# Kernel tuning notes

Measured on AMD Instinct MI355X. Metric: run time of the kernel, lower is better.

The kernel has to match this reference:

```python
import jax, jax.numpy as jnp
import numpy as np

N_NODES = 100000
N_EDGES = 3200000
N_GRAPHS = 1024
IN_DIM, HID, OUT = 1, 32, 32
BN_EPS = 1e-5


def setup_inputs() -> dict:
    key = jax.random.key(0)
    ks = jax.random.split(key, 12)
    inp = {
        "x": jax.random.normal(ks[0], (N_NODES, IN_DIM), dtype=jnp.float32),
        "edge_index": jax.random.randint(ks[1], (2, N_EDGES), 0, N_NODES, dtype=jnp.int64),
        "batch": jnp.sort(jax.random.randint(ks[2], (N_NODES,), 0, N_GRAPHS, dtype=jnp.int64)),
        # GCNConv linear weights (out = x @ W + b) and BatchNorm (eval-mode) params
        "W1": jax.random.normal(ks[3], (IN_DIM, HID), dtype=jnp.float32) / np.sqrt(IN_DIM),
        "b1": jnp.zeros((HID,), jnp.float32),
        "bn1_g": jnp.ones((HID,), jnp.float32),
        "bn1_b": jnp.zeros((HID,), jnp.float32),
        "bn1_m": jax.random.normal(ks[4], (HID,), dtype=jnp.float32) * 0.1,
        "bn1_v": jnp.ones((HID,), jnp.float32),
        "W2": jax.random.normal(ks[5], (HID, HID), dtype=jnp.float32) / np.sqrt(HID),
        "b2": jnp.zeros((HID,), jnp.float32),
        "bn2_g": jnp.ones((HID,), jnp.float32),
        "bn2_b": jnp.zeros((HID,), jnp.float32),
        "bn2_m": jax.random.normal(ks[6], (HID,), dtype=jnp.float32) * 0.1,
        "bn2_v": jnp.ones((HID,), jnp.float32),
        "W3": jax.random.normal(ks[7], (HID, OUT), dtype=jnp.float32) / np.sqrt(HID),
        "b3": jnp.zeros((OUT,), jnp.float32),
    }
    return inp


def _gcn_norm(edge_index, n_nodes):
    # add self loops, compute sym-normalized edge weights (PyG GCNConv default)
    loop = jnp.arange(n_nodes, dtype=edge_index.dtype)
    src = jnp.concatenate([edge_index[0], loop])
    dst = jnp.concatenate([edge_index[1], loop])
    deg = jax.ops.segment_sum(jnp.ones_like(dst, dtype=jnp.float32), dst, num_segments=n_nodes)
    dinv = jnp.where(deg > 0, jax.lax.rsqrt(deg), 0.0)
    norm = dinv[src] * dinv[dst]  # [E + N]
    return src, dst, norm


def _gcn_conv(x, src, dst, norm, W, b, n_nodes):
    h = x @ W                                   # [N, F_out]
    msg = h[src] * norm[:, None]                # gather + scale, [E+N, F_out]
    out = jax.ops.segment_sum(msg, dst, num_segments=n_nodes)  # scatter-add
    return out + b


def _bn_eval(x, g, b, m, v):
    return (x - m) * jax.lax.rsqrt(v + BN_EPS) * g + b


def reference(x, edge_index, batch, W1, b1, bn1_g, bn1_b, bn1_m, bn1_v,
              W2, b2, bn2_g, bn2_b, bn2_m, bn2_v, W3, b3):
    n = x.shape[0]
    src, dst, norm = _gcn_norm(edge_index, n)
    h = _gcn_conv(x, src, dst, norm, W1, b1, n)
    h = jax.nn.relu(_bn_eval(h, bn1_g, bn1_b, bn1_m, bn1_v))  # dropout = id (eval)
    h = _gcn_conv(h, src, dst, norm, W2, b2, n)
    h = jax.nn.relu(_bn_eval(h, bn2_g, bn2_b, bn2_m, bn2_v))
    h = _gcn_conv(h, src, dst, norm, W3, b3, n)
    # global mean pool over graphs
    sums = jax.ops.segment_sum(h, batch, num_segments=N_GRAPHS)
    cnts = jax.ops.segment_sum(jnp.ones((n,), h.dtype), batch, num_segments=N_GRAPHS)
    return sums / jnp.maximum(cnts, 1.0)[:, None]
```

## Files before the change

### kernel.cpp

```cpp
#include <hip/hip_runtime.h>

#define N_NODES 100000
#define N_EDGES 3200000
#define N_GRAPHS 1024
#define HID 32
#define BN_EPS 1e-5f
#define NB 256

#define NBKT 512
#define NPB 196
#define PART_TILE 4096
#define PART_THREADS 256
#define PART_EPT (PART_TILE / PART_THREADS)

#define G2_NODES 8
#define G2_WCAP 2048


__device__ __forceinline__ int lbound(const int* __restrict__ a, int n, int key) {
    int lo = 0, hi = n;
    while (lo < hi) {
        int mid = (lo + hi) >> 1;
        if (a[mid] < key) lo = mid + 1; else hi = mid;
    }
    return lo;
}

__device__ __forceinline__ float bf2f(unsigned short h) {
    return __uint_as_float((unsigned)h << 16);
}
__device__ __forceinline__ unsigned short f2bf(float x) {
    unsigned u = __float_as_uint(x);
    u += 0x7fffu + ((u >> 16) & 1u);
    return (unsigned short)(u >> 16);
}


__global__ void k_zero(int* __restrict__ bhist) {
    bhist[threadIdx.x] = 0;
}

__global__ void k_hist(const int* __restrict__ dst, int* __restrict__ bhist) {
    __shared__ int h[NBKT];
    for (int i = threadIdx.x; i < NBKT; i += NB) h[i] = 0;
    __syncthreads();
    for (int e = blockIdx.x * NB + threadIdx.x; e < N_EDGES; e += gridDim.x * NB)
        atomicAdd(&h[__builtin_nontemporal_load(&dst[e]) / NPB], 1);
    __syncthreads();
    for (int i = threadIdx.x; i < NBKT; i += NB)
        if (h[i]) atomicAdd(&bhist[i], h[i]);
}

__global__ void k_scan512(const int* __restrict__ bhist, int* __restrict__ bstart,
                          int* __restrict__ bcursor) {
    __shared__ int sm[NBKT];
    int t = threadIdx.x;
    int orig = bhist[t];
    sm[t] = orig;
    __syncthreads();
    for (int off = 1; off < NBKT; off <<= 1) {
        int v = (t >= off) ? sm[t - off] : 0;
        __syncthreads();
        sm[t] += v;
        __syncthreads();
    }
    int ex = sm[t] - orig;
    bstart[t] = ex;
    bcursor[t] = ex;
    if (t == NBKT - 1) bstart[NBKT] = sm[t];
}

__global__ void k_partition(const int* __restrict__ src, const int* __restrict__ dst,
                            int* __restrict__ bcursor, unsigned* __restrict__ ebuf) {
    __shared__ int lh[NBKT];
    __shared__ int lcur[NBKT];
    const int tile0 = blockIdx.x * PART_TILE;
    for (int i = threadIdx.x; i < NBKT; i += PART_THREADS) lh[i] = 0;
    __syncthreads();
    int s[PART_EPT], bk[PART_EPT], dl[PART_EPT];
#pragma unroll
    for (int k = 0; k < PART_EPT; ++k) {
        int e = tile0 + k * PART_THREADS + threadIdx.x;
        bool ok = (e < N_EDGES);
        int sv = ok ? __builtin_nontemporal_load(&src[e]) : 0;
        int dv = ok ? __builtin_nontemporal_load(&dst[e]) : 0;
        s[k] = sv;
        bk[k] = ok ? (dv / NPB) : -1;
        dl[k] = dv - bk[k] * NPB;
        if (ok) atomicAdd(&lh[bk[k]], 1);
    }
    __syncthreads();
    for (int i = threadIdx.x; i < NBKT; i += PART_THREADS)
        lcur[i] = lh[i] ? atomicAdd(&bcursor[i], lh[i]) : 0;
    __syncthreads();
#pragma unroll
    for (int k = 0; k < PART_EPT; ++k) {
        if (bk[k] >= 0) {
            int pos = atomicAdd(&lcur[bk[k]], 1);
            ebuf[pos] = ((unsigned)dl[k] << 17) | (unsigned)s[k];
        }
    }
}

__global__ void k_bucket(const int* __restrict__ bstart,
                         const unsigned* __restrict__ ebuf,
                         const float* __restrict__ x,
                         int* __restrict__ rowstart, int* __restrict__ deg,
                         float* __restrict__ dinv, float* __restrict__ zs1,
                         int* __restrict__ csr) {
    __shared__ int hist[NPB];
    __shared__ int sm[256];
    __shared__ int lcur[NPB];
    const int b = blockIdx.x;
    const int node0 = b * NPB;
    const int nn = N_NODES - node0;
    const int elo = bstart[b], ehi = bstart[b + 1];
    const int t = threadIdx.x;

    for (int i = t; i < NPB; i += blockDim.x) hist[i] = 0;
    __syncthreads();
    for (int e = elo + t; e < ehi; e += blockDim.x)
        atomicAdd(&hist[ebuf[e] >> 17], 1);
    __syncthreads();
    int orig = 0;
    if (t < 256) { orig = (t < NPB) ? hist[t] : 0; sm[t] = orig; }
    __syncthreads();
    for (int off = 1; off < 256; off <<= 1) {
        int v = 0;
        if (t < 256 && t >= off) v = sm[t - off];
        __syncthreads();
        if (t < 256) sm[t] += v;
        __syncthreads();
    }
    if (t < NPB) {
        int ex = sm[t] - orig;
        lcur[t] = ex;
        if (t < nn) {
            int node = node0 + t;
            rowstart[node] = elo + ex;
            deg[node] = orig;
            float di = rsqrtf((float)(orig + 1));
            dinv[node] = di;
            zs1[node] = di * x[node];
        }
    }
    __syncthreads();
    for (int e = elo + t; e < ehi; e += blockDim.x) {
        unsigned pk = ebuf[e];
        int pos = atomicAdd(&lcur[pk >> 17], 1);
        csr[elo + pos] = (int)(pk & 0x1FFFFu);
    }
}


__global__ void k_gather1(const int* __restrict__ rowstart, const int* __restrict__ deg,
                          const int* __restrict__ csr, const float* __restrict__ dinv,
                          const float* __restrict__ zs1, float2* __restrict__ sd) {
    int v = blockIdx.x * NB + threadIdx.x;
    if (v < N_NODES) {
        int lo = rowstart[v], n = deg[v];
        float acc = zs1[v];
        int j = 0;
        for (; j + 4 <= n; j += 4) {
            int u0 = __builtin_nontemporal_load(&csr[lo + j]);
            int u1 = __builtin_nontemporal_load(&csr[lo + j + 1]);
            int u2 = __builtin_nontemporal_load(&csr[lo + j + 2]);
            int u3 = __builtin_nontemporal_load(&csr[lo + j + 3]);
            float a0 = zs1[u0], a1 = zs1[u1], a2 = zs1[u2], a3 = zs1[u3];
            acc += (a0 + a1) + (a2 + a3);
        }
        for (; j < n; ++j) acc += zs1[csr[lo + j]];
        float di = dinv[v];
        sd[v] = make_float2(di * acc, di);
    }
}

__global__ void k_gather2(const int* __restrict__ rowstart, const int* __restrict__ deg,
                          const int* __restrict__ csr, const float2* __restrict__ sd,
                          const float* __restrict__ W1, const float* __restrict__ b1,
                          const float* __restrict__ g1, const float* __restrict__ bb1,
                          const float* __restrict__ m1, const float* __restrict__ v1,
                          const float* __restrict__ W2,
                          const float* __restrict__ b2, const float* __restrict__ g2,
                          const float* __restrict__ bb2, const float* __restrict__ m2,
                          const float* __restrict__ v2,
                          unsigned short* __restrict__ zs3a,
                          unsigned short* __restrict__ zs3b) {
    __shared__ float Ws[HID * HID];
    __shared__ float2 sde[G2_WCAP];
    __shared__ float rowbuf[G2_NODES][HID + 1];
    __shared__ int sb[2];
    const int tid = threadIdx.x;
    for (int k = tid; k < HID * HID; k += NB) Ws[k] = W2[k];

    const int r = tid >> 5, f = tid & 31;
    const int v = blockIdx.x * G2_NODES + r;
    const bool valid = v < N_NODES;

    if (tid == 0) {
        int first = blockIdx.x * G2_NODES;
        int last = min(first + G2_NODES - 1, N_NODES - 1);
        sb[0] = rowstart[first];
        sb[1] = rowstart[last] + deg[last];
    }

    const float sc1 = g1[f] * rsqrtf(v1[f] + BN_EPS);
    const float A = W1[f] * sc1;
    const float Bc = (b1[f] - m1[f]) * sc1 + bb1[f];

    float di = 0.0f, acc = 0.0f;
    int rs = 0, re = 0;
    if (valid) {
        rs = rowstart[v];
        re = rs + deg[v];
        float2 pv = sd[v];
        di = pv.y;
        acc = di * fmaxf(pv.x * A + Bc, 0.0f);
    }
    __syncthreads();
    const int blo = sb[0], bhi = sb[1];

    for (int w = blo; w < bhi; w += G2_WCAP) {
        const int wn = min(G2_WCAP, bhi - w);
        for (int i = tid; i < wn; i += NB) {
            int u = __builtin_nontemporal_load(&csr[w + i]);
            sde[i] = sd[u];
        }
        __syncthreads();
        int jlo = max(rs, w) - w;
        int jhi = min(re, w + wn) - w;
        int j = jlo;
        for (; j + 4 <= jhi; j += 4) {
            float2 p0 = sde[j], p1 = sde[j + 1], p2 = sde[j + 2], p3 = sde[j + 3];
            float a0 = p0.y * fmaxf(p0.x * A + Bc, 0.0f);
            float a1 = p1.y * fmaxf(p1.x * A + Bc, 0.0f);
            float a2 = p2.y * fmaxf(p2.x * A + Bc, 0.0f);
            float a3 = p3.y * fmaxf(p3.x * A + Bc, 0.0f);
            acc += (a0 + a1) + (a2 + a3);
        }
        for (; j < jhi; ++j) {
            float2 p = sde[j];
            acc += p.y * fmaxf(p.x * A + Bc, 0.0f);
        }
        __syncthreads();
    }
    acc *= di;
    rowbuf[r][f] = acc;
    __syncthreads();
    if (valid) {
        float h = b2[f];
#pragma unroll
        for (int k = 0; k < HID; ++k) h += rowbuf[r][k] * Ws[k * HID + f];
        float sc2 = g2[f] * rsqrtf(v2[f] + BN_EPS);
        float z = fmaxf((h - m2[f]) * sc2 + bb2[f], 0.0f);
        unsigned short o = f2bf(di * z);
        if (f < 16) zs3a[v * 16 + f] = o;
        else        zs3b[v * 16 + (f - 16)] = o;
    }
}


__global__ void k_gather3h(const int* __restrict__ rowstart, const int* __restrict__ deg,
                           const int* __restrict__ csr, const float* __restrict__ dinv,
                           const unsigned short* __restrict__ tab,
                           unsigned short* __restrict__ agg3h, int halfofs) {
    int t = blockIdx.x * NB + threadIdx.x;
    int v = t >> 4, f = t & 15;
    if (v < N_NODES) {
        int lo = rowstart[v], n = deg[v];
        float acc = bf2f(tab[v * 16 + f]);
        int j = 0;
        for (; j + 8 <= n; j += 8) {
            int u0 = __builtin_nontemporal_load(&csr[lo + j]);
            int u1 = __builtin_nontemporal_load(&csr[lo + j + 1]);
            int u2 = __builtin_nontemporal_load(&csr[lo + j + 2]);
            int u3 = __builtin_nontemporal_load(&csr[lo + j + 3]);
            int u4 = __builtin_nontemporal_load(&csr[lo + j + 4]);
            int u5 = __builtin_nontemporal_load(&csr[lo + j + 5]);
            int u6 = __builtin_nontemporal_load(&csr[lo + j + 6]);
            int u7 = __builtin_nontemporal_load(&csr[lo + j + 7]);
            float a0 = bf2f(tab[u0 * 16 + f]);
            float a1 = bf2f(tab[u1 * 16 + f]);
            float a2 = bf2f(tab[u2 * 16 + f]);
            float a3 = bf2f(tab[u3 * 16 + f]);
            float a4 = bf2f(tab[u4 * 16 + f]);
            float a5 = bf2f(tab[u5 * 16 + f]);
            float a6 = bf2f(tab[u6 * 16 + f]);
            float a7 = bf2f(tab[u7 * 16 + f]);
            acc += ((a0 + a1) + (a2 + a3)) + ((a4 + a5) + (a6 + a7));
        }
        for (; j < n; ++j) acc += bf2f(tab[csr[lo + j] * 16 + f]);
        __builtin_nontemporal_store(f2bf(dinv[v] * acc), &agg3h[v * HID + halfofs + f]);
    }
}


__global__ void k_pool(const unsigned short* __restrict__ agg3h,
                       const int* __restrict__ batch,
                       const float* __restrict__ W3, const float* __restrict__ b3,
                       float* __restrict__ out) {
    __shared__ float Ws[HID * HID];
    __shared__ float part[NB / HID][HID + 1];
    __shared__ float mrow[HID];
    int g = blockIdx.x;
    for (int k = threadIdx.x; k < HID * HID; k += NB) Ws[k] = W3[k];

    int lo = lbound(batch, N_NODES, g);
    int hi = lbound(batch, N_NODES, g + 1);

    int r = threadIdx.x >> 5, f = threadIdx.x & 31;
    float acc = 0.0f;
    for (int i = lo + r; i < hi; i += NB / HID)
        acc += bf2f(__builtin_nontemporal_load(&agg3h[i * HID + f]));
    part[r][f] = acc;
    __syncthreads();
    if (threadIdx.x < HID) {
        float srow = 0.0f;
#pragma unroll
        for (int k = 0; k < NB / HID; ++k) srow += part[k][threadIdx.x];
        float c = (float)(hi - lo);
        mrow[threadIdx.x] = (hi > lo) ? srow / c : 0.0f;
    }
    __syncthreads();
    if (threadIdx.x < HID) {
        int ff = threadIdx.x;
        float o = 0.0f;
        if (hi > lo) {
            o = b3[ff];
#pragma unroll
            for (int k = 0; k < HID; ++k) o += mrow[k] * Ws[k * HID + ff];
        }
        out[g * HID + ff] = o;
    }
}


extern "C" void kernel_launch(void* const* d_in, const int* in_sizes, int n_in,
                              void* d_out, int out_size, void* d_ws, size_t ws_size,
                              hipStream_t stream) {
    const float* x     = (const float*)d_in[0];
    const int*   eidx  = (const int*)d_in[1];
    const int*   batch = (const int*)d_in[2];
    const float* W1    = (const float*)d_in[3];
    const float* b1    = (const float*)d_in[4];
    const float* bn1g  = (const float*)d_in[5];
    const float* bn1b  = (const float*)d_in[6];
    const float* bn1m  = (const float*)d_in[7];
    const float* bn1v  = (const float*)d_in[8];
    const float* W2    = (const float*)d_in[9];
    const float* b2    = (const float*)d_in[10];
    const float* bn2g  = (const float*)d_in[11];
    const float* bn2b  = (const float*)d_in[12];
    const float* bn2m  = (const float*)d_in[13];
    const float* bn2v  = (const float*)d_in[14];
    const float* W3    = (const float*)d_in[15];
    const float* b3    = (const float*)d_in[16];
    float* out = (float*)d_out;

    const int* src = eidx;
    const int* dst = eidx + N_EDGES;

    char* ws = (char*)d_ws;
    size_t off = 0;
    auto carve = [&](size_t bytes) {
        void* p = ws + off;
        off += (bytes + 255) & ~size_t(255);
        return p;
    };
    int*    bhist    = (int*)carve(NBKT * 4);
    int*    bstart   = (int*)carve((NBKT + 1) * 4);
    int*    bcursor  = (int*)carve(NBKT * 4);
    int*    rowstart = (int*)carve(N_NODES * 4);
    int*    deg      = (int*)carve(N_NODES * 4);
    float*  dinv     = (float*)carve(N_NODES * 4);
    float*  zs1      = (float*)carve(N_NODES * 4);
    float2* sd       = (float2*)carve((size_t)N_NODES * 8);
    int*    csr      = (int*)carve((size_t)N_EDGES * 4);
    char*   region   = (char*)carve((size_t)N_EDGES * 4);
    unsigned*       ebuf  = (unsigned*)region;
    unsigned short* zs3a  = (unsigned short*)region;
    unsigned short* zs3b  = (unsigned short*)(region + (size_t)N_NODES * 16 * 2);
    unsigned short* agg3h = (unsigned short*)(region + (size_t)N_NODES * 32 * 2);

    const int gN    = (N_NODES + NB - 1) / NB;
    const int gG2   = (N_NODES + G2_NODES - 1) / G2_NODES;
    const int gG3   = (N_NODES * 16 + NB - 1) / NB;
    const int gPart = (N_EDGES + PART_TILE - 1) / PART_TILE;

    k_zero<<<1, NBKT, 0, stream>>>(bhist);
    k_hist<<<1024, NB, 0, stream>>>(dst, bhist);
    k_scan512<<<1, NBKT, 0, stream>>>(bhist, bstart, bcursor);
    k_partition<<<gPart, PART_THREADS, 0, stream>>>(src, dst, bcursor, ebuf);
    k_bucket<<<NBKT, 512, 0, stream>>>(bstart, ebuf, x, rowstart, deg, dinv, zs1, csr);
    k_gather1<<<gN, NB, 0, stream>>>(rowstart, deg, csr, dinv, zs1, sd);
    k_gather2<<<gG2, NB, 0, stream>>>(rowstart, deg, csr, sd,
                                      W1, b1, bn1g, bn1b, bn1m, bn1v,
                                      W2, b2, bn2g, bn2b, bn2m, bn2v, zs3a, zs3b);
    k_gather3h<<<gG3, NB, 0, stream>>>(rowstart, deg, csr, dinv, zs3a, agg3h, 0);
    k_gather3h<<<gG3, NB, 0, stream>>>(rowstart, deg, csr, dinv, zs3b, agg3h, 16);
    k_pool<<<N_GRAPHS, NB, 0, stream>>>(agg3h, batch, W3, b3, out);
}
```

Measured before the change: 267.4 us.

## Split edge lists across sub-groups per node in gather2 and gather3h

In k_gather2 each node now gets a full 64-lane wavefront instead of 32 threads, with the two half-waves splitting the node's edges and the 32x32 matvec. The partials are combined with a cross-lane shuffle, and the edge window and nodes per block are halved. In k_gather3h each node gets a 64-lane wavefront where four 16-lane groups stride the edge list, and the partials are reduced with shuffles. The aim is to shorten per-thread serial loops over edges and put more independent loads in flight, in exchange for four times as many blocks and some reduction overhead.

```diff
diff --git a/kernel.cpp b/kernel.cpp
--- a/kernel.cpp
+++ b/kernel.cpp
@@ -13,8 +13,8 @@
 #define PART_THREADS 256
 #define PART_EPT (PART_TILE / PART_THREADS)
 
-#define G2_NODES 8
-#define G2_WCAP 2048
+#define G2_NODES 4
+#define G2_WCAP 1024
 
 
 __device__ __forceinline__ int lbound(const int* __restrict__ a, int n, int key) {
@@ -193,7 +193,10 @@
     const int tid = threadIdx.x;
     for (int k = tid; k < HID * HID; k += NB) Ws[k] = W2[k];
 
-    const int r = tid >> 5, f = tid & 31;
+    const int r = tid >> 6;
+    const int lane = tid & 63;
+    const int f = lane & 31;
+    const int esub = lane >> 5;
     const int v = blockIdx.x * G2_NODES + r;
     const bool valid = v < N_NODES;
 
@@ -215,7 +218,7 @@
         re = rs + deg[v];
         float2 pv = sd[v];
         di = pv.y;
-        acc = di * fmaxf(pv.x * A + Bc, 0.0f);
+        if (esub == 0) acc = di * fmaxf(pv.x * A + Bc, 0.0f);
     }
     __syncthreads();
     const int blo = sb[0], bhi = sb[1];
@@ -229,28 +232,34 @@
         __syncthreads();
         int jlo = max(rs, w) - w;
         int jhi = min(re, w + wn) - w;
-        int j = jlo;
-        for (; j + 4 <= jhi; j += 4) {
-            float2 p0 = sde[j], p1 = sde[j + 1], p2 = sde[j + 2], p3 = sde[j + 3];
-            float a0 = p0.y * fmaxf(p0.x * A + Bc, 0.0f);
-            float a1 = p1.y * fmaxf(p1.x * A + Bc, 0.0f);
-            float a2 = p2.y * fmaxf(p2.x * A + Bc, 0.0f);
-            float a3 = p3.y * fmaxf(p3.x * A + Bc, 0.0f);
-            acc += (a0 + a1) + (a2 + a3);
-        }
-        for (; j < jhi; ++j) {
-            float2 p = sde[j];
-            acc += p.y * fmaxf(p.x * A + Bc, 0.0f);
-        }
-        __syncthreads();
-    }
+        int jb = jlo;
+        for (; jb + 4 <= jhi; jb += 4) {
+            float2 p0 = sde[jb + esub];
+            float2 p1 = sde[jb + 2 + esub];
+            acc += p0.y * fmaxf(p0.x * A + Bc, 0.0f);
+            acc += p1.y * fmaxf(p1.x * A + Bc, 0.0f);
+        }
+        for (; jb < jhi; jb += 2) {
+            int j = jb + esub;
+            if (j < jhi) {
+                float2 p = sde[j];
+                acc += p.y * fmaxf(p.x * A + Bc, 0.0f);
+            }
+        }
+        __syncthreads();
+    }
+    acc += __shfl_xor(acc, 32, 64);
     acc *= di;
-    rowbuf[r][f] = acc;
-    __syncthreads();
-    if (valid) {
-        float h = b2[f];
+    if (lane < 32) rowbuf[r][f] = acc;
+    __syncthreads();
+
+    float hp = 0.0f;
+    const int k0 = esub * 16;
 #pragma unroll
-        for (int k = 0; k < HID; ++k) h += rowbuf[r][k] * Ws[k * HID + f];
+    for (int k = 0; k < 16; ++k) hp += rowbuf[r][k0 + k] * Ws[(k0 + k) * HID + f];
+    hp += __shfl_xor(hp, 32, 64);
+    if (valid && lane < 32) {
+        float h = b2[f] + hp;
         float sc2 = g2[f] * rsqrtf(v2[f] + BN_EPS);
         float z = fmaxf((h - m2[f]) * sc2 + bb2[f], 0.0f);
         unsigned short o = f2bf(di * z);
@@ -259,38 +268,45 @@
     }
 }
 
-
 __global__ void k_gather3h(const int* __restrict__ rowstart, const int* __restrict__ deg,
                            const int* __restrict__ csr, const float* __restrict__ dinv,
                            const unsigned short* __restrict__ tab,
                            unsigned short* __restrict__ agg3h, int halfofs) {
-    int t = blockIdx.x * NB + threadIdx.x;
-    int v = t >> 4, f = t & 15;
-    if (v < N_NODES) {
-        int lo = rowstart[v], n = deg[v];
-        float acc = bf2f(tab[v * 16 + f]);
-        int j = 0;
-        for (; j + 8 <= n; j += 8) {
-            int u0 = __builtin_nontemporal_load(&csr[lo + j]);
-            int u1 = __builtin_nontemporal_load(&csr[lo + j + 1]);
-            int u2 = __builtin_nontemporal_load(&csr[lo + j + 2]);
-            int u3 = __builtin_nontemporal_load(&csr[lo + j + 3]);
-            int u4 = __builtin_nontemporal_load(&csr[lo + j + 4]);
-            int u5 = __builtin_nontemporal_load(&csr[lo + j + 5]);
-            int u6 = __builtin_nontemporal_load(&csr[lo + j + 6]);
-            int u7 = __builtin_nontemporal_load(&csr[lo + j + 7]);
-            float a0 = bf2f(tab[u0 * 16 + f]);
-            float a1 = bf2f(tab[u1 * 16 + f]);
-            float a2 = bf2f(tab[u2 * 16 + f]);
-            float a3 = bf2f(tab[u3 * 16 + f]);
-            float a4 = bf2f(tab[u4 * 16 + f]);
-            float a5 = bf2f(tab[u5 * 16 + f]);
-            float a6 = bf2f(tab[u6 * 16 + f]);
-            float a7 = bf2f(tab[u7 * 16 + f]);
-            acc += ((a0 + a1) + (a2 + a3)) + ((a4 + a5) + (a6 + a7));
-        }
-        for (; j < n; ++j) acc += bf2f(tab[csr[lo + j] * 16 + f]);
-        __builtin_nontemporal_store(f2bf(dinv[v] * acc), &agg3h[v * HID + halfofs + f]);
+    const int tid = threadIdx.x;
+    const int lane = tid & 63;
+    const int f = lane & 15;
+    const int esub = lane >> 4;
+    const int v = blockIdx.x * 4 + (tid >> 6);
+    if (v >= N_NODES) return;
+
+    const int lo = rowstart[v], n = deg[v];
+    float acc = 0.0f;
+    int jb = 0;
+    for (; jb + 16 <= n; jb += 16) {
+        int j0 = jb + esub, j1 = jb + 4 + esub, j2 = jb + 8 + esub, j3 = jb + 12 + esub;
+        int u0 = __builtin_nontemporal_load(&csr[lo + j0]);
+        int u1 = __builtin_nontemporal_load(&csr[lo + j1]);
+        int u2 = __builtin_nontemporal_load(&csr[lo + j2]);
+        int u3 = __builtin_nontemporal_load(&csr[lo + j3]);
+        float a0 = bf2f(tab[u0 * 16 + f]);
+        float a1 = bf2f(tab[u1 * 16 + f]);
+        float a2 = bf2f(tab[u2 * 16 + f]);
+        float a3 = bf2f(tab[u3 * 16 + f]);
+        acc += (a0 + a1) + (a2 + a3);
+    }
+    for (; jb < n; jb += 4) {
+        int j = jb + esub;
+        if (j < n) {
+            int u = __builtin_nontemporal_load(&csr[lo + j]);
+            acc += bf2f(tab[u * 16 + f]);
+        }
+    }
+    acc += __shfl_xor(acc, 16, 64);
+    acc += __shfl_xor(acc, 32, 64);
+    if (esub == 0) {
+        acc += bf2f(tab[v * 16 + f]);
+        __builtin_nontemporal_store(f2bf(dinv[v] * acc),
+                                    &agg3h[v * HID + halfofs + f]);
     }
 }
 
@@ -384,7 +400,7 @@
 
     const int gN    = (N_NODES + NB - 1) / NB;
     const int gG2   = (N_NODES + G2_NODES - 1) / G2_NODES;
-    const int gG3   = (N_NODES * 16 + NB - 1) / NB;
+    const int gG3   = (N_NODES + 3) / 4;
     const int gPart = (N_EDGES + PART_TILE - 1) / PART_TILE;
 
     k_zero<<<1, NBKT, 0, stream>>>(bhist);
```

Result: slower. 315.4 us (+17.9%).
